# Optimization experiments

Measured on AMD Instinct MI355X. Metric: run time of the kernel, lower is better.

## Reference

```python
import jax, jax.numpy as jnp
import numpy as np

ALPHA = 10.0
BETA = 0.05
FAR_DELTA = 1e10  # matches torch 10000000000.0 padding for the last delta


def sdf_to_density(signed_distance, alpha, beta):
    s = -signed_distance
    return jnp.where(
        s <= 0,
        alpha * (0.5 * jnp.exp(s / beta)),
        alpha * (1.0 - 0.5 * jnp.exp(-s / beta)),
    )


def setup_inputs() -> dict:
    key = jax.random.key(0)
    k1, k2, k3 = jax.random.split(key, 3)
    R, N = 65536, 128
    distance = jax.random.normal(k1, (R, N), dtype=jnp.float32)  # SDF values
    color = jax.random.uniform(k2, (R, N, 3), dtype=jnp.float32)
    # per-ray sorted sample depths in [2, 6] (near/far)
    t = jax.random.uniform(k3, (R, N), dtype=jnp.float32)
    depth_values = jnp.sort(2.0 + 4.0 * t, axis=-1)
    return {"distance": distance, "color": color, "depth_values": depth_values}


def reference(distance, color, depth_values):
    # deltas: [R, N], last delta padded with a huge value
    deltas = jnp.concatenate(
        [depth_values[:, 1:] - depth_values[:, :-1],
         jnp.full_like(depth_values[:, :1], FAR_DELTA)],
        axis=-1,
    )
    density = sdf_to_density(distance, ALPHA, BETA)  # [R, N]
    d = density * deltas  # [R, N]
    # transmittance: exp(-cumsum of previous densities), exclusive scan
    trans = jnp.exp(-jnp.concatenate(
        [jnp.zeros_like(d[:, :1]), jnp.cumsum(d[:, :-1], axis=-1)], axis=-1))
    weights = (1.0 - jnp.exp(-d)) * trans  # [R, N]
    out_color = jnp.sum(weights[..., None] * color, axis=-2)  # [R, 3]
    geometry = jnp.zeros_like(color)  # faithful to geometry_color = zeros_like(color)
    return out_color, geometry
```

## Files before the change

### kernel.cpp

```cpp
#include <hip/hip_runtime.h>

#define ALPHA     10.0f
#define INV_BETA  20.0f
#define FAR_DELTA 1e10f
#define NSAMP     128

__device__ __forceinline__ float laplace_density(float sdf) {
    float s = -sdf;
    float e = __expf(-fabsf(s) * INV_BETA);
    return (s <= 0.f) ? (0.5f * ALPHA * e) : (ALPHA * (1.f - 0.5f * e));
}

__global__ __launch_bounds__(256) void volsdf_render(
    const float* __restrict__ dist,
    const float* __restrict__ color,
    const float* __restrict__ depth,
    float*       __restrict__ out,
    int R)
{
    const int lane   = threadIdx.x & 63;
    const int waveId = threadIdx.x >> 6;
    const int sub    = lane & 31;
    const int half   = lane >> 5;
    const int rayPair = blockIdx.x * 4 + waveId;
    const int ray     = rayPair * 2 + half;
    if (ray >= R) return;

    const size_t rbase = (size_t)ray * NSAMP;

    float4 di = ((const float4*)(dist  + rbase))[sub];
    float4 dp = ((const float4*)(depth + rbase))[sub];
    const float* cp = color + rbase * 3 + (size_t)sub * 12;
    float4 c0 = ((const float4*)cp)[0];
    float4 c1 = ((const float4*)cp)[1];
    float4 c2 = ((const float4*)cp)[2];

    float nx  = __shfl_down(dp.x, 1, 32);
    float dl0 = dp.y - dp.x;
    float dl1 = dp.z - dp.y;
    float dl2 = dp.w - dp.z;
    float dl3 = (sub == 31) ? FAR_DELTA : (nx - dp.w);

    float d0 = laplace_density(di.x) * dl0;
    float d1 = laplace_density(di.y) * dl1;
    float d2 = laplace_density(di.z) * dl2;
    float d3 = laplace_density(di.w) * dl3;

    float local = (d0 + d1) + (d2 + d3);
    float incl  = local;
    #pragma unroll
    for (int off = 1; off < 32; off <<= 1) {
        float v = __shfl_up(incl, off, 32);
        if (sub >= off) incl += v;
    }
    float base = __shfl_up(incl, 1, 32);
    if (sub == 0) base = 0.f;

    float p1 = base + d0, p2 = p1 + d1, p3 = p2 + d2;
    float w0 = (1.f - __expf(-d0)) * __expf(-base);
    float w1 = (1.f - __expf(-d1)) * __expf(-p1);
    float w2 = (1.f - __expf(-d2)) * __expf(-p2);
    float w3 = (1.f - __expf(-d3)) * __expf(-p3);

    float ar = (w0 * c0.x + w1 * c0.w) + (w2 * c1.z + w3 * c2.y);
    float ag = (w0 * c0.y + w1 * c1.x) + (w2 * c1.w + w3 * c2.z);
    float ab = (w0 * c0.z + w1 * c1.y) + (w2 * c2.x + w3 * c2.w);

    #pragma unroll
    for (int off = 16; off > 0; off >>= 1) {
        ar += __shfl_down(ar, off, 32);
        ag += __shfl_down(ag, off, 32);
        ab += __shfl_down(ab, off, 32);
    }
    if (sub == 0) {
        out[(size_t)ray * 3 + 0] = ar;
        out[(size_t)ray * 3 + 1] = ag;
        out[(size_t)ray * 3 + 2] = ab;
    }
}

extern "C" void kernel_launch(void* const* d_in, const int* in_sizes, int n_in,
                              void* d_out, int out_size, void* d_ws, size_t ws_size,
                              hipStream_t stream) {
    const float* dist  = (const float*)d_in[0];
    const float* color = (const float*)d_in[1];
    const float* depth = (const float*)d_in[2];
    float* out = (float*)d_out;

    const int R = in_sizes[0] / NSAMP;
    const int blocks = (R + 7) / 8;

    hipMemsetAsync(d_out, 0, (size_t)out_size * sizeof(float), stream);

    hipLaunchKernelGGL(volsdf_render, dim3(blocks), dim3(256), 0, stream,
                       dist, color, depth, out, R);
}
```

Baseline: 223.9 us.

## Switch to one-thread-per-ray sequential compositing with LDS-staged chunked loads

Replaces the half-wave-per-ray layout, with its shuffle-based prefix scan and reduction, by one thread per ray that composites samples sequentially, carrying transmittance multiplicatively. Input chunks of 8 samples for 256 rays are loaded coalesced into LDS, and the next chunk's global loads are issued into registers before the current chunk is processed, giving software prefetch. This removes the cross-lane scan and reduction and the per-sample exp of a prefix sum. The cost is 16 barrier-separated chunk iterations, higher LDS use per block and far fewer blocks (256 for 65536 rays), which may leave many CUs with little to overlap memory latency.

```diff
diff --git a/kernel.cpp b/kernel.cpp
--- a/kernel.cpp
+++ b/kernel.cpp
@@ -4,12 +4,11 @@
 #define INV_BETA  20.0f
 #define FAR_DELTA 1e10f
 #define NSAMP     128
-
-__device__ __forceinline__ float laplace_density(float sdf) {
-    float s = -sdf;
-    float e = __expf(-fabsf(s) * INV_BETA);
-    return (s <= 0.f) ? (0.5f * ALPHA * e) : (ALPHA * (1.f - 0.5f * e));
-}
+#define CH        8
+#define NCHUNK    (NSAMP/CH)
+#define RPB       256
+#define SD_STRIDE 12
+#define SC_STRIDE 28
 
 __global__ __launch_bounds__(256) void volsdf_render(
     const float* __restrict__ dist,
@@ -18,65 +17,101 @@
     float*       __restrict__ out,
     int R)
 {
-    const int lane   = threadIdx.x & 63;
-    const int waveId = threadIdx.x >> 6;
-    const int sub    = lane & 31;
-    const int half   = lane >> 5;
-    const int rayPair = blockIdx.x * 4 + waveId;
-    const int ray     = rayPair * 2 + half;
-    if (ray >= R) return;
+    __shared__ float sd[RPB * SD_STRIDE];
+    __shared__ float sp[RPB * SD_STRIDE];
+    __shared__ float sc[RPB * SC_STRIDE];
 
-    const size_t rbase = (size_t)ray * NSAMP;
+    const int t  = threadIdx.x;
+    const int R0 = blockIdx.x * RPB;
+    if (R0 >= R) return;
 
-    float4 di = ((const float4*)(dist  + rbase))[sub];
-    float4 dp = ((const float4*)(depth + rbase))[sub];
-    const float* cp = color + rbase * 3 + (size_t)sub * 12;
-    float4 c0 = ((const float4*)cp)[0];
-    float4 c1 = ((const float4*)cp)[1];
-    float4 c2 = ((const float4*)cp)[2];
+    const float4* gd = (const float4*)dist;
+    const float4* gp = (const float4*)depth;
+    const float4* gc = (const float4*)color;
 
-    float nx  = __shfl_down(dp.x, 1, 32);
-    float dl0 = dp.y - dp.x;
-    float dl1 = dp.z - dp.y;
-    float dl2 = dp.w - dp.z;
-    float dl3 = (sub == 31) ? FAR_DELTA : (nx - dp.w);
+    float4 pd0, pd1, pp0, pp1, pc0, pc1, pc2, pc3, pc4, pc5;
 
-    float d0 = laplace_density(di.x) * dl0;
-    float d1 = laplace_density(di.y) * dl1;
-    float d2 = laplace_density(di.z) * dl2;
-    float d3 = laplace_density(di.w) * dl3;
+    const int ray0 = t >> 1;
+    const int pos0 = t & 1;
 
-    float local = (d0 + d1) + (d2 + d3);
-    float incl  = local;
-    #pragma unroll
-    for (int off = 1; off < 32; off <<= 1) {
-        float v = __shfl_up(incl, off, 32);
-        if (sub >= off) incl += v;
+    auto issue_loads = [&](int c) {
+        size_t b0 = (size_t)(R0 + ray0) * 32 + c * 2 + pos0;
+        size_t b1 = (size_t)(R0 + 128 + ray0) * 32 + c * 2 + pos0;
+        pd0 = gd[b0];  pd1 = gd[b1];
+        pp0 = gp[b0];  pp1 = gp[b1];
+        #pragma unroll
+        for (int k = 0; k < 6; ++k) {
+            int q = t + 256 * k;
+            int ray = q / 6, pos = q % 6;
+            float4 v = gc[(size_t)(R0 + ray) * 96 + c * 6 + pos];
+            if (k == 0) pc0 = v; else if (k == 1) pc1 = v; else if (k == 2) pc2 = v;
+            else if (k == 3) pc3 = v; else if (k == 4) pc4 = v; else pc5 = v;
+        }
+    };
+
+    auto write_lds = [&]() {
+        *(float4*)&sd[ray0 * SD_STRIDE + pos0 * 4]         = pd0;
+        *(float4*)&sd[(128 + ray0) * SD_STRIDE + pos0 * 4] = pd1;
+        *(float4*)&sp[ray0 * SD_STRIDE + pos0 * 4]         = pp0;
+        *(float4*)&sp[(128 + ray0) * SD_STRIDE + pos0 * 4] = pp1;
+        #pragma unroll
+        for (int k = 0; k < 6; ++k) {
+            int q = t + 256 * k;
+            int ray = q / 6, pos = q % 6;
+            float4 v = (k == 0) ? pc0 : (k == 1) ? pc1 : (k == 2) ? pc2
+                     : (k == 3) ? pc3 : (k == 4) ? pc4 : pc5;
+            *(float4*)&sc[ray * SC_STRIDE + pos * 4] = v;
+        }
+    };
+
+    float tr = 1.f, aR = 0.f, aG = 0.f, aB = 0.f;
+    float carD = 0.f, carR = 0.f, carG = 0.f, carB = 0.f, carP = 0.f;
+
+    auto proc = [&](float sdf, float cr, float cg, float cb, float delta) {
+        float s = -sdf;
+        float e = __expf(-fabsf(s) * INV_BETA);
+        float dens = (s <= 0.f) ? (0.5f * ALPHA * e) : (ALPHA * (1.f - 0.5f * e));
+        float dd = dens * delta;
+        float ee = __expf(-dd);
+        float w  = tr * (1.f - ee);
+        aR += w * cr; aG += w * cg; aB += w * cb;
+        tr *= ee;
+    };
+
+    issue_loads(0);
+    for (int c = 0; c < NCHUNK; ++c) {
+        if (c) __syncthreads();
+        write_lds();
+        __syncthreads();
+        if (c + 1 < NCHUNK) issue_loads(c + 1);
+
+        float4 d0 = *(const float4*)&sd[t * SD_STRIDE];
+        float4 d1 = *(const float4*)&sd[t * SD_STRIDE + 4];
+        float4 p0 = *(const float4*)&sp[t * SD_STRIDE];
+        float4 p1 = *(const float4*)&sp[t * SD_STRIDE + 4];
+        float cb_[24];
+        *(float4*)&cb_[0]  = *(const float4*)&sc[t * SC_STRIDE];
+        *(float4*)&cb_[4]  = *(const float4*)&sc[t * SC_STRIDE + 4];
+        *(float4*)&cb_[8]  = *(const float4*)&sc[t * SC_STRIDE + 8];
+        *(float4*)&cb_[12] = *(const float4*)&sc[t * SC_STRIDE + 12];
+        *(float4*)&cb_[16] = *(const float4*)&sc[t * SC_STRIDE + 16];
+        *(float4*)&cb_[20] = *(const float4*)&sc[t * SC_STRIDE + 20];
+
+        float ds_[8] = { d0.x, d0.y, d0.z, d0.w, d1.x, d1.y, d1.z, d1.w };
+        float pp_[8] = { p0.x, p0.y, p0.z, p0.w, p1.x, p1.y, p1.z, p1.w };
+
+        if (c) proc(carD, carR, carG, carB, pp_[0] - carP);
+        #pragma unroll
+        for (int s = 0; s < 7; ++s)
+            proc(ds_[s], cb_[s*3], cb_[s*3+1], cb_[s*3+2], pp_[s+1] - pp_[s]);
+        carD = ds_[7]; carR = cb_[21]; carG = cb_[22]; carB = cb_[23]; carP = pp_[7];
     }
-    float base = __shfl_up(incl, 1, 32);
-    if (sub == 0) base = 0.f;
+    proc(carD, carR, carG, carB, FAR_DELTA);
 
-    float p1 = base + d0, p2 = p1 + d1, p3 = p2 + d2;
-    float w0 = (1.f - __expf(-d0)) * __expf(-base);
-    float w1 = (1.f - __expf(-d1)) * __expf(-p1);
-    float w2 = (1.f - __expf(-d2)) * __expf(-p2);
-    float w3 = (1.f - __expf(-d3)) * __expf(-p3);
-
-    float ar = (w0 * c0.x + w1 * c0.w) + (w2 * c1.z + w3 * c2.y);
-    float ag = (w0 * c0.y + w1 * c1.x) + (w2 * c1.w + w3 * c2.z);
-    float ab = (w0 * c0.z + w1 * c1.y) + (w2 * c2.x + w3 * c2.w);
-
-    #pragma unroll
-    for (int off = 16; off > 0; off >>= 1) {
-        ar += __shfl_down(ar, off, 32);
-        ag += __shfl_down(ag, off, 32);
-        ab += __shfl_down(ab, off, 32);
-    }
-    if (sub == 0) {
-        out[(size_t)ray * 3 + 0] = ar;
-        out[(size_t)ray * 3 + 1] = ag;
-        out[(size_t)ray * 3 + 2] = ab;
-    }
+    const size_t ray = (size_t)(R0 + t);
+    out[ray * 3 + 0] = aR;
+    out[ray * 3 + 1] = aG;
+    out[ray * 3 + 2] = aB;
 }
 
 extern "C" void kernel_launch(void* const* d_in, const int* in_sizes, int n_in,
@@ -88,7 +123,7 @@
     float* out = (float*)d_out;
 
     const int R = in_sizes[0] / NSAMP;
-    const int blocks = (R + 7) / 8;
+    const int blocks = (R + RPB - 1) / RPB;
 
     hipMemsetAsync(d_out, 0, (size_t)out_size * sizeof(float), stream);
 
```

Measured after the change: 233.6 us. 1.04x slower.
